# Kernel tuning notes

Hardware: AMD Instinct MI355X
Metric: run time of the kernel (lower is better)

## Reference

```python
import jax, jax.numpy as jnp
import numpy as np

B = 4096
I = 2048  # input_size
H = 2048  # hidden_size


def setup_inputs() -> dict:
    key = jax.random.key(0)
    ks = jax.random.split(key, 5)
    # xavier-uniform-ish scale for the stacked weights (fan_in=2048, fan_out=2048)
    w_scale = np.sqrt(2.0 / (I + H)).astype(np.float32)
    return {
        "x": jax.random.normal(ks[0], (B, I), dtype=jnp.float32),
        "h": jax.random.normal(ks[1], (B, H), dtype=jnp.float32),
        "c": jax.random.normal(ks[2], (B, H), dtype=jnp.float32),
        # stacked gate weights in order [i, f, g, o], each block [H, in]
        "W_x": jax.random.normal(ks[3], (4 * H, I), dtype=jnp.float32) * w_scale,
        "b_x": jnp.zeros((4 * H,), dtype=jnp.float32),
        "W_h": jax.random.normal(ks[4], (4 * H, H), dtype=jnp.float32) * w_scale,
        "b_h": jnp.zeros((4 * H,), dtype=jnp.float32),
    }


def reference(x, h, c, W_x, b_x, W_h, b_h):
    # Two fused GEMMs replace the 8 per-gate nn.Linear calls (same math).
    gates = (
        jnp.einsum("bi,gi->bg", x, W_x)
        + jnp.einsum("bh,gh->bg", h, W_h)
        + b_x
        + b_h
    )  # [B, 4H], gate order i, f, g, o
    i_t, f_t, g_t, o_t = jnp.split(gates, 4, axis=-1)
    i_t = jax.nn.sigmoid(i_t)
    f_t = jax.nn.sigmoid(f_t)
    o_t = jax.nn.sigmoid(o_t)
    g_t = jnp.tanh(g_t)
    c_new = f_t * c + i_t * g_t
    h_new = o_t * jnp.tanh(c_new)
    return (h_new, c_new)
```

## Files before the change

### kernel.cpp

```cpp
#include <hip/hip_runtime.h>
#include <hip/hip_bf16.h>
#include <stdint.h>


typedef float        f32x4 __attribute__((ext_vector_type(4)));
typedef short        s16x8 __attribute__((ext_vector_type(8)));
typedef unsigned int u32x4 __attribute__((ext_vector_type(4)));
typedef unsigned int u32x2 __attribute__((ext_vector_type(2)));
typedef unsigned short ushort_t;

#define BH_TOT 8388608
#define NT 128
#define ALO_B 33554432
#define WLO_B 67108864

__device__ __forceinline__ void splitf4(f32x4 v, u32x2& hp, u32x2& lp) {
  unsigned int u0 = __float_as_uint(v[0]), u1 = __float_as_uint(v[1]);
  unsigned int u2 = __float_as_uint(v[2]), u3 = __float_as_uint(v[3]);
  float d0 = v[0] - __uint_as_float(u0 & 0xFFFF0000u);
  float d1 = v[1] - __uint_as_float(u1 & 0xFFFF0000u);
  float d2 = v[2] - __uint_as_float(u2 & 0xFFFF0000u);
  float d3 = v[3] - __uint_as_float(u3 & 0xFFFF0000u);
  hp[0] = (u0 >> 16) | (u1 & 0xFFFF0000u);
  hp[1] = (u2 >> 16) | (u3 & 0xFFFF0000u);
  unsigned int l0 = __float_as_uint(d0), l1 = __float_as_uint(d1);
  unsigned int l2 = __float_as_uint(d2), l3 = __float_as_uint(d3);
  lp[0] = (l0 >> 16) | (l1 & 0xFFFF0000u);
  lp[1] = (l2 >> 16) | (l3 & 0xFFFF0000u);
}

__device__ __forceinline__ float sigmoidf_(float x) {
  return 1.0f / (1.0f + __expf(-x));
}

__global__ __launch_bounds__(256) void conv_split(
    const float* __restrict__ src, ushort_t* __restrict__ dhi,
    ushort_t* __restrict__ dlo, int n4, int colOff) {
  const int stride = gridDim.x * blockDim.x;
  for (int i = blockIdx.x * blockDim.x + threadIdx.x; i < n4; i += stride) {
    const int row = i >> 9;
    const int c4 = (i & 511) << 2;
    f32x4 v = *(const f32x4*)(src + ((size_t)i << 2));
    u32x2 hp, lp;
    splitf4(v, hp, lp);
    const size_t off = (size_t)row * 4096 + colOff + c4;
    *(u32x2*)(dhi + off) = hp;
    *(u32x2*)(dlo + off) = lp;
  }
}

__device__ __forceinline__ void glds16(const void* g, void* l) {
  __builtin_amdgcn_global_load_lds(
      (const __attribute__((address_space(1))) unsigned int*)g,
      (__attribute__((address_space(3))) unsigned int*)l, 16, 0, 0);
}

__device__ __forceinline__ s16x8 ldfrag(const ushort_t* plane, int row, int kq) {
  const int slot = kq ^ (row & 3);
  return *(const s16x8*)(plane + row * 32 + slot * 8);
}

#define VMCNT4 asm volatile("s_waitcnt vmcnt(4)" ::: "memory")
#define BARRIER asm volatile("s_barrier" ::: "memory")

#define MFMA16(A_, B_, R_)                                                  \
  do {                                                                      \
    __builtin_amdgcn_s_setprio(1);                                          \
    _Pragma("unroll") for (int tm_ = 0; tm_ < 4; ++tm_)                     \
        _Pragma("unroll") for (int tn_ = 0; tn_ < 4; ++tn_)                 \
            acc[(R_) + tm_][tn_] = __builtin_amdgcn_mfma_f32_16x16x32_bf16( \
                A_[tm_], B_[tn_], acc[(R_) + tm_][tn_], 0, 0, 0);           \
    __builtin_amdgcn_s_setprio(0);                                          \
  } while (0)

#define GLA(extra, plo)                                        \
  do {                                                         \
    glds16(srcA0 + (extra) + ko, bn_ + (plo) + wld);           \
    glds16(srcA1 + (extra) + ko, bn_ + (plo) + 8192 + wld);    \
  } while (0)
#define GLW(extra, plo)                                        \
  do {                                                         \
    glds16(srcW0 + (extra) + ko, bn_ + (plo) + wld);           \
    glds16(srcW1 + (extra) + ko, bn_ + (plo) + 8192 + wld);    \
  } while (0)

__global__ __launch_bounds__(512, 2) void lstm_gemm(
    const ushort_t* __restrict__ Whi, const ushort_t* __restrict__ Ahi,
    const float* __restrict__ cold, const float* __restrict__ bx,
    const float* __restrict__ bh, float* __restrict__ out) {
  __shared__ unsigned char smem[131072];

  const int tid = threadIdx.x;
  const int lane = tid & 63;
  const int wid = tid >> 6;
  const int wg = wid & 3;
  const int wm = wid >> 2;
  const int m16 = lane & 15;
  const int kq = lane >> 4;

  const int swz = (blockIdx.x & 7) * 64 + (blockIdx.x >> 3);
  const int bm0 = (swz >> 5) * 256;
  const int col0 = (swz & 31) * 64;

  const int lrow = tid >> 2;
  const int lslot = tid & 3;
  const int gsl = (lslot ^ (lrow & 3)) << 4;
  const char* Ab = (const char*)Ahi;
  const char* Wb = (const char*)Whi;
  const char* srcA0 = Ab + (size_t)(bm0 + lrow) * 8192 + gsl;
  const char* srcA1 = Ab + (size_t)(bm0 + 128 + lrow) * 8192 + gsl;
  const int wr0 = (lrow >> 6) * 2048 + col0 + (lrow & 63);
  const int wr1 = wr0 + 2 * 2048;
  const char* srcW0 = Wb + (size_t)wr0 * 8192 + gsl;
  const char* srcW1 = Wb + (size_t)wr1 * 8192 + gsl;

  const int wld = wid * 1024;

  f32x4 acc[8][4] = {};

  {
    unsigned char* bn_ = smem;
    const int ko = 0;
    GLA(0, 0);
    GLW(0, 32768);
    GLA(ALO_B, 16384);
    GLW(WLO_B, 49152);
  }
  VMCNT4;
  BARRIER;

  for (int t = 0; t < NT; ++t) {
    const int cb = t & 1;
    unsigned char* bc_ = smem + cb * 65536;
    unsigned char* bn_ = smem + (cb ^ 1) * 65536;
    const int ktn = (t + 1 < NT) ? t + 1 : t;
    const int ko = ktn << 6;
    const ushort_t* pAh = (const ushort_t*)(bc_);
    const ushort_t* pAl = (const ushort_t*)(bc_ + 16384);
    const ushort_t* pWh = (const ushort_t*)(bc_ + 32768);
    const ushort_t* pWl = (const ushort_t*)(bc_ + 49152);
    const int ra = wm * 128;
    s16x8 wh[4], wl[4], a0[4], a1[4];

#pragma unroll
    for (int i = 0; i < 4; ++i) wh[i] = ldfrag(pWh, wg * 64 + i * 16 + m16, kq);
#pragma unroll
    for (int i = 0; i < 4; ++i) a0[i] = ldfrag(pAh, ra + i * 16 + m16, kq);
    GLA(0, 0);
    VMCNT4;
    BARRIER;
    MFMA16(a0, wh, 0);
    BARRIER;

#pragma unroll
    for (int i = 0; i < 4; ++i) a1[i] = ldfrag(pAl, ra + i * 16 + m16, kq);
    GLW(0, 32768);
    VMCNT4;
    BARRIER;
    MFMA16(a1, wh, 0);
    BARRIER;

#pragma unroll
    for (int i = 0; i < 4; ++i) wl[i] = ldfrag(pWl, wg * 64 + i * 16 + m16, kq);
    GLA(ALO_B, 16384);
    BARRIER;
    MFMA16(a0, wl, 0);
    BARRIER;

#pragma unroll
    for (int i = 0; i < 4; ++i)
      a0[i] = ldfrag(pAh, ra + 64 + i * 16 + m16, kq);
    GLW(WLO_B, 49152);
    BARRIER;
    MFMA16(a0, wh, 4);
    BARRIER;

#pragma unroll
    for (int i = 0; i < 4; ++i)
      a1[i] = ldfrag(pAl, ra + 64 + i * 16 + m16, kq);
    BARRIER;
    MFMA16(a1, wh, 4);
    BARRIER;

    VMCNT4;
    BARRIER;
    MFMA16(a0, wl, 4);
    BARRIER;
  }

  __syncthreads();
  float* gl = (float*)smem;
  const int colg = tid & 15;
  const int rr = tid >> 4;
  const int cgl = col0 + colg * 4;
  f32x4 bi = *(const f32x4*)(bx + cgl) + *(const f32x4*)(bh + cgl);
  f32x4 bf_ = *(const f32x4*)(bx + 2048 + cgl) + *(const f32x4*)(bh + 2048 + cgl);
  f32x4 bg = *(const f32x4*)(bx + 4096 + cgl) + *(const f32x4*)(bh + 4096 + cgl);
  f32x4 bo = *(const f32x4*)(bx + 6144 + cgl) + *(const f32x4*)(bh + 6144 + cgl);

#pragma unroll
  for (int hh = 0; hh < 2; ++hh) {
    if (hh) __syncthreads();
    if (wm == hh) {
#pragma unroll
      for (int tm = 0; tm < 8; ++tm)
#pragma unroll
        for (int tn = 0; tn < 4; ++tn) {
          const int r = tm * 16 + kq * 4;
          const int c = tn * 16 + m16;
#pragma unroll
          for (int i = 0; i < 4; ++i)
            gl[wg * 8192 + (r + i) * 64 + c] = acc[tm][tn][i];
        }
    }
    __syncthreads();
#pragma unroll
    for (int j = 0; j < 4; ++j) {
      const int r = rr + j * 32;
      f32x4 gi = *(const f32x4*)&gl[0 * 8192 + r * 64 + colg * 4] + bi;
      f32x4 gf = *(const f32x4*)&gl[1 * 8192 + r * 64 + colg * 4] + bf_;
      f32x4 gg = *(const f32x4*)&gl[2 * 8192 + r * 64 + colg * 4] + bg;
      f32x4 go = *(const f32x4*)&gl[3 * 8192 + r * 64 + colg * 4] + bo;
      const size_t gbase = (size_t)(bm0 + hh * 128 + r) * 2048 + cgl;
      f32x4 cv = *(const f32x4*)(cold + gbase);
      f32x4 cn, hn;
#pragma unroll
      for (int e = 0; e < 4; ++e) {
        float iv = sigmoidf_(gi[e]);
        float fv = sigmoidf_(gf[e]);
        float gv = tanhf(gg[e]);
        float ov = sigmoidf_(go[e]);
        float c2 = fv * cv[e] + iv * gv;
        cn[e] = c2;
        hn[e] = ov * tanhf(c2);
      }
      *(f32x4*)(out + gbase) = hn;
      *(f32x4*)(out + BH_TOT + gbase) = cn;
    }
  }
}

__device__ __forceinline__ void splitw(f32x4 w0, f32x4 w1, s16x8& hi, s16x8& lo) {
  u32x2 h0, l0, h1, l1;
  splitf4(w0, h0, l0);
  splitf4(w1, h1, l1);
  u32x4 hu = {h0[0], h0[1], h1[0], h1[1]};
  u32x4 lu = {l0[0], l0[1], l1[0], l1[1]};
  hi = __builtin_bit_cast(s16x8, hu);
  lo = __builtin_bit_cast(s16x8, lu);
}

__global__ __launch_bounds__(256, 2) void lstm_fused(
    const float* __restrict__ x, const float* __restrict__ h,
    const float* __restrict__ cold, const float* __restrict__ Wx,
    const float* __restrict__ bx, const float* __restrict__ Wh,
    const float* __restrict__ bh, float* __restrict__ out) {
  __shared__ unsigned char smem[69632];
  ushort_t* Ah = (ushort_t*)smem;
  ushort_t* Al = (ushort_t*)(smem + 5120);
  float* gl = (float*)smem;

  const int tid = threadIdx.x;
  const int lane = tid & 63;
  const int wid = tid >> 6;

  const int swz = (blockIdx.x & 7) * 256 + (blockIdx.x >> 3);
  const int bn = swz >> 6;
  const int bm = swz & 63;
  const int row0 = bm * 64;
  const int col0 = bn * 64;

  const int ar0 = tid >> 3;
  const int akc = (tid & 7) << 2;
  const int wcol = lane & 15;
  const int kch = (lane >> 4) << 3;

  f32x4 acc[4][4];
#pragma unroll
  for (int i = 0; i < 4; ++i)
#pragma unroll
    for (int j = 0; j < 4; ++j) acc[i][j] = (f32x4)0.0f;

#pragma unroll
  for (int ph = 0; ph < 2; ++ph) {
    const float* Ap = ph ? h : x;
    const float* Wp = ph ? Wh : Wx;
    const float* arow0 = Ap + (size_t)(row0 + ar0) * 2048 + akc;
    const float* arow1 = arow0 + 32 * 2048;
    const float* wb[4];
#pragma unroll
    for (int tn = 0; tn < 4; ++tn)
      wb[tn] = Wp + (size_t)(wid * 2048 + col0 + tn * 16 + wcol) * 2048 + kch;

    f32x4 a0 = *(const f32x4*)(arow0);
    f32x4 a1 = *(const f32x4*)(arow1);

    for (int kt = 0; kt < 64; ++kt) {
      const int k0 = kt << 5;
      f32x4 wr[4][2];
#pragma unroll
      for (int tn = 0; tn < 4; ++tn) {
        wr[tn][0] = *(const f32x4*)(wb[tn] + k0);
        wr[tn][1] = *(const f32x4*)(wb[tn] + k0 + 4);
      }
      {
        u32x2 hp, lp;
        splitf4(a0, hp, lp);
        *(u32x2*)(Ah + ar0 * 40 + akc) = hp;
        *(u32x2*)(Al + ar0 * 40 + akc) = lp;
        splitf4(a1, hp, lp);
        *(u32x2*)(Ah + (ar0 + 32) * 40 + akc) = hp;
        *(u32x2*)(Al + (ar0 + 32) * 40 + akc) = lp;
      }
      __syncthreads();
      if (kt != 63) {
        a0 = *(const f32x4*)(arow0 + k0 + 32);
        a1 = *(const f32x4*)(arow1 + k0 + 32);
      }
      s16x8 ah[4], al[4];
#pragma unroll
      for (int tm = 0; tm < 4; ++tm) {
        const int off = (tm * 16 + wcol) * 40 + kch;
        ah[tm] = *(const s16x8*)(Ah + off);
        al[tm] = *(const s16x8*)(Al + off);
      }
      s16x8 whh[4], wll[4];
#pragma unroll
      for (int tn = 0; tn < 4; ++tn) splitw(wr[tn][0], wr[tn][1], whh[tn], wll[tn]);
#pragma unroll
      for (int tm = 0; tm < 4; ++tm)
#pragma unroll
        for (int tn = 0; tn < 4; ++tn)
          acc[tm][tn] = __builtin_amdgcn_mfma_f32_16x16x32_bf16(
              ah[tm], whh[tn], acc[tm][tn], 0, 0, 0);
#pragma unroll
      for (int tm = 0; tm < 4; ++tm)
#pragma unroll
        for (int tn = 0; tn < 4; ++tn)
          acc[tm][tn] = __builtin_amdgcn_mfma_f32_16x16x32_bf16(
              ah[tm], wll[tn], acc[tm][tn], 0, 0, 0);
#pragma unroll
      for (int tm = 0; tm < 4; ++tm)
#pragma unroll
        for (int tn = 0; tn < 4; ++tn)
          acc[tm][tn] = __builtin_amdgcn_mfma_f32_16x16x32_bf16(
              al[tm], whh[tn], acc[tm][tn], 0, 0, 0);
      __syncthreads();
    }
  }

  {
    const int rbase = (lane >> 4) << 2;
#pragma unroll
    for (int tm = 0; tm < 4; ++tm)
#pragma unroll
      for (int tn = 0; tn < 4; ++tn) {
        const int r = tm * 16 + rbase;
        const int cc = tn * 16 + wcol;
#pragma unroll
        for (int i = 0; i < 4; ++i)
          gl[wid * 4352 + (r + i) * 68 + cc] = acc[tm][tn][i];
      }
  }
  __syncthreads();

  const int ecol = (tid & 15) << 2;
  const int er0 = tid >> 4;
  const int cg = col0 + ecol;
  f32x4 bi = *(const f32x4*)(bx + cg) + *(const f32x4*)(bh + cg);
  f32x4 bf = *(const f32x4*)(bx + 2048 + cg) + *(const f32x4*)(bh + 2048 + cg);
  f32x4 bg = *(const f32x4*)(bx + 4096 + cg) + *(const f32x4*)(bh + 4096 + cg);
  f32x4 bo = *(const f32x4*)(bx + 6144 + cg) + *(const f32x4*)(bh + 6144 + cg);
#pragma unroll
  for (int j = 0; j < 4; ++j) {
    const int r = er0 + j * 16;
    const size_t gbase = (size_t)(row0 + r) * 2048 + cg;
    f32x4 gi = *(const f32x4*)&gl[0 * 4352 + r * 68 + ecol] + bi;
    f32x4 gf = *(const f32x4*)&gl[1 * 4352 + r * 68 + ecol] + bf;
    f32x4 gg = *(const f32x4*)&gl[2 * 4352 + r * 68 + ecol] + bg;
    f32x4 go = *(const f32x4*)&gl[3 * 4352 + r * 68 + ecol] + bo;
    f32x4 cv = *(const f32x4*)(cold + gbase);
    f32x4 cn, hn;
#pragma unroll
    for (int e = 0; e < 4; ++e) {
      float iv = sigmoidf_(gi[e]);
      float fv = sigmoidf_(gf[e]);
      float gv = tanhf(gg[e]);
      float ov = sigmoidf_(go[e]);
      float c2 = fv * cv[e] + iv * gv;
      cn[e] = c2;
      hn[e] = ov * tanhf(c2);
    }
    *(f32x4*)(out + gbase) = hn;
    *(f32x4*)(out + BH_TOT + gbase) = cn;
  }
}

extern "C" void kernel_launch(void* const* d_in, const int* in_sizes, int n_in,
                              void* d_out, int out_size, void* d_ws,
                              size_t ws_size, hipStream_t stream) {
  const float* x = (const float*)d_in[0];
  const float* h = (const float*)d_in[1];
  const float* c = (const float*)d_in[2];
  const float* Wx = (const float*)d_in[3];
  const float* bx = (const float*)d_in[4];
  const float* Wh = (const float*)d_in[5];
  const float* bh = (const float*)d_in[6];
  float* out = (float*)d_out;

  const size_t NEED = 201326592ULL;
  if (ws_size >= NEED) {
    ushort_t* base = (ushort_t*)d_ws;
    ushort_t* Whi = base;
    ushort_t* Wlo = base + 33554432;
    ushort_t* Ahi = base + 67108864;
    ushort_t* Alo = base + 83886080;
    hipLaunchKernelGGL(conv_split, dim3(4096), dim3(256), 0, stream, Wx, Whi,
                       Wlo, 8192 * 512, 0);
    hipLaunchKernelGGL(conv_split, dim3(4096), dim3(256), 0, stream, Wh, Whi,
                       Wlo, 8192 * 512, 2048);
    hipLaunchKernelGGL(conv_split, dim3(2048), dim3(256), 0, stream, x, Ahi,
                       Alo, 4096 * 512, 0);
    hipLaunchKernelGGL(conv_split, dim3(2048), dim3(256), 0, stream, h, Ahi,
                       Alo, 4096 * 512, 2048);
    hipLaunchKernelGGL(lstm_gemm, dim3(512), dim3(512), 0, stream, Whi, Ahi, c,
                       bx, bh, out);
  } else {
    hipLaunchKernelGGL(lstm_fused, dim3(2048), dim3(256), 0, stream, x, h, c,
                       Wx, bx, Wh, bh, out);
  }
}
```

Before: 921.8 us.

## Merge split-conversion launches, change LDS swizzle, cluster MFMAs with fewer barriers

```diff
diff --git a/kernel.cpp b/kernel.cpp
--- a/kernel.cpp
+++ b/kernel.cpp
@@ -33,19 +33,26 @@
   return 1.0f / (1.0f + __expf(-x));
 }
 
-__global__ __launch_bounds__(256) void conv_split(
-    const float* __restrict__ src, ushort_t* __restrict__ dhi,
-    ushort_t* __restrict__ dlo, int n4, int colOff) {
+__global__ __launch_bounds__(256) void conv_split2(
+    const float* __restrict__ srcA, const float* __restrict__ srcB,
+    ushort_t* __restrict__ dhi, ushort_t* __restrict__ dlo, int nGroups) {
   const int stride = gridDim.x * blockDim.x;
-  for (int i = blockIdx.x * blockDim.x + threadIdx.x; i < n4; i += stride) {
-    const int row = i >> 9;
-    const int c4 = (i & 511) << 2;
-    f32x4 v = *(const f32x4*)(src + ((size_t)i << 2));
-    u32x2 hp, lp;
-    splitf4(v, hp, lp);
-    const size_t off = (size_t)row * 4096 + colOff + c4;
-    *(u32x2*)(dhi + off) = hp;
-    *(u32x2*)(dlo + off) = lp;
+  for (int g = blockIdx.x * blockDim.x + threadIdx.x; g < nGroups; g += stride) {
+    const int row = g >> 9;
+    const int gi = g & 511;
+    const int half = gi >> 8;
+    const int c8 = (gi & 255) << 3;
+    const float* s = (half ? srcB : srcA) + (size_t)row * 2048 + c8;
+    f32x4 v0 = *(const f32x4*)s;
+    f32x4 v1 = *(const f32x4*)(s + 4);
+    u32x2 h0, l0, h1, l1;
+    splitf4(v0, h0, l0);
+    splitf4(v1, h1, l1);
+    u32x4 hv = {h0[0], h0[1], h1[0], h1[1]};
+    u32x4 lv = {l0[0], l0[1], l1[0], l1[1]};
+    const size_t off = (size_t)row * 4096 + half * 2048 + c8;
+    *(u32x4*)(dhi + off) = hv;
+    *(u32x4*)(dlo + off) = lv;
   }
 }
 
@@ -56,21 +63,27 @@
 }
 
 __device__ __forceinline__ s16x8 ldfrag(const ushort_t* plane, int row, int kq) {
-  const int slot = kq ^ (row & 3);
+  const int slot = kq ^ ((row >> 1) & 3);
   return *(const s16x8*)(plane + row * 32 + slot * 8);
 }
 
-#define VMCNT4 asm volatile("s_waitcnt vmcnt(4)" ::: "memory")
+#define VMCNT2 asm volatile("s_waitcnt vmcnt(2)" ::: "memory")
 #define BARRIER asm volatile("s_barrier" ::: "memory")
 
 #define MFMA16(A_, B_, R_)                                                  \
   do {                                                                      \
-    __builtin_amdgcn_s_setprio(1);                                          \
     _Pragma("unroll") for (int tm_ = 0; tm_ < 4; ++tm_)                     \
         _Pragma("unroll") for (int tn_ = 0; tn_ < 4; ++tn_)                 \
             acc[(R_) + tm_][tn_] = __builtin_amdgcn_mfma_f32_16x16x32_bf16( \
                 A_[tm_], B_[tn_], acc[(R_) + tm_][tn_], 0, 0, 0);           \
-    __builtin_amdgcn_s_setprio(0);                                          \
+  } while (0)
+
+#define CLUSTER(A1_, B1_, R1_, A2_, B2_, R2_) \
+  do {                                        \
+    __builtin_amdgcn_s_setprio(1);            \
+    MFMA16(A1_, B1_, R1_);                    \
+    MFMA16(A2_, B2_, R2_);                    \
+    __builtin_amdgcn_s_setprio(0);            \
   } while (0)
 
 #define GLA(extra, plo)                                        \
@@ -104,7 +117,7 @@
 
   const int lrow = tid >> 2;
   const int lslot = tid & 3;
-  const int gsl = (lslot ^ (lrow & 3)) << 4;
+  const int gsl = (lslot ^ ((lrow >> 1) & 3)) << 4;
   const char* Ab = (const char*)Ahi;
   const char* Wb = (const char*)Whi;
   const char* srcA0 = Ab + (size_t)(bm0 + lrow) * 8192 + gsl;
@@ -126,7 +139,7 @@
     GLA(ALO_B, 16384);
     GLW(WLO_B, 49152);
   }
-  VMCNT4;
+  VMCNT2;
   BARRIER;
 
   for (int t = 0; t < NT; ++t) {
@@ -140,51 +153,38 @@
     const ushort_t* pWh = (const ushort_t*)(bc_ + 32768);
     const ushort_t* pWl = (const ushort_t*)(bc_ + 49152);
     const int ra = wm * 128;
-    s16x8 wh[4], wl[4], a0[4], a1[4];
+    s16x8 wh[4], wl[4], a0[4], a1[4], a0p[4], a1p[4];
 
 #pragma unroll
     for (int i = 0; i < 4; ++i) wh[i] = ldfrag(pWh, wg * 64 + i * 16 + m16, kq);
 #pragma unroll
     for (int i = 0; i < 4; ++i) a0[i] = ldfrag(pAh, ra + i * 16 + m16, kq);
+#pragma unroll
+    for (int i = 0; i < 4; ++i) a1[i] = ldfrag(pAl, ra + i * 16 + m16, kq);
     GLA(0, 0);
-    VMCNT4;
-    BARRIER;
-    MFMA16(a0, wh, 0);
-    BARRIER;
-
-#pragma unroll
-    for (int i = 0; i < 4; ++i) a1[i] = ldfrag(pAl, ra + i * 16 + m16, kq);
+    VMCNT2;
+    BARRIER;
+    CLUSTER(a0, wh, 0, a1, wh, 0);
+    BARRIER;
+
+#pragma unroll
+    for (int i = 0; i < 4; ++i) wl[i] = ldfrag(pWl, wg * 64 + i * 16 + m16, kq);
+#pragma unroll
+    for (int i = 0; i < 4; ++i)
+      a0p[i] = ldfrag(pAh, ra + 64 + i * 16 + m16, kq);
     GLW(0, 32768);
-    VMCNT4;
-    BARRIER;
-    MFMA16(a1, wh, 0);
-    BARRIER;
-
-#pragma unroll
-    for (int i = 0; i < 4; ++i) wl[i] = ldfrag(pWl, wg * 64 + i * 16 + m16, kq);
     GLA(ALO_B, 16384);
     BARRIER;
-    MFMA16(a0, wl, 0);
+    CLUSTER(a0, wl, 0, a0p, wh, 4);
     BARRIER;
 
 #pragma unroll
     for (int i = 0; i < 4; ++i)
-      a0[i] = ldfrag(pAh, ra + 64 + i * 16 + m16, kq);
+      a1p[i] = ldfrag(pAl, ra + 64 + i * 16 + m16, kq);
     GLW(WLO_B, 49152);
-    BARRIER;
-    MFMA16(a0, wh, 4);
-    BARRIER;
-
-#pragma unroll
-    for (int i = 0; i < 4; ++i)
-      a1[i] = ldfrag(pAl, ra + 64 + i * 16 + m16, kq);
-    BARRIER;
-    MFMA16(a1, wh, 4);
-    BARRIER;
-
-    VMCNT4;
-    BARRIER;
-    MFMA16(a0, wl, 4);
+    VMCNT2;
+    BARRIER;
+    CLUSTER(a1p, wh, 4, a0p, wl, 4);
     BARRIER;
   }
 
@@ -415,14 +415,10 @@
     ushort_t* Wlo = base + 33554432;
     ushort_t* Ahi = base + 67108864;
     ushort_t* Alo = base + 83886080;
-    hipLaunchKernelGGL(conv_split, dim3(4096), dim3(256), 0, stream, Wx, Whi,
-                       Wlo, 8192 * 512, 0);
-    hipLaunchKernelGGL(conv_split, dim3(4096), dim3(256), 0, stream, Wh, Whi,
-                       Wlo, 8192 * 512, 2048);
-    hipLaunchKernelGGL(conv_split, dim3(2048), dim3(256), 0, stream, x, Ahi,
-                       Alo, 4096 * 512, 0);
-    hipLaunchKernelGGL(conv_split, dim3(2048), dim3(256), 0, stream, h, Ahi,
-                       Alo, 4096 * 512, 2048);
+    hipLaunchKernelGGL(conv_split2, dim3(4096), dim3(256), 0, stream, Wx, Wh,
+                       Whi, Wlo, 8192 * 512);
+    hipLaunchKernelGGL(conv_split2, dim3(2048), dim3(256), 0, stream, x, h,
+                       Ahi, Alo, 4096 * 512);
     hipLaunchKernelGGL(lstm_gemm, dim3(512), dim3(512), 0, stream, Whi, Ahi, c,
                        bx, bh, out);
   } else {
```

New measurement: 893.1 us. -3.1%, faster.
